# Optimization experiments

Hardware: AMD Instinct MI355X
Metric: run time of the kernel (lower is better)

The kernel has to match this reference:

```python
import jax, jax.numpy as jnp
import numpy as np

N_IN = 28
N_MID = 256
N_OUT = 28
SEQ = 28
BATCH = 4096


def setup_inputs() -> dict:
    key = jax.random.key(0)
    ks = jax.random.split(key, 8)
    s_ih = 1.0 / np.sqrt(N_MID)
    x = jax.random.normal(ks[0], (BATCH, SEQ, N_IN), dtype=jnp.float32)
    # PyTorch nn.GRU params: weight_ih_l0 [3H, in], weight_hh_l0 [3H, H], biases [3H]
    w_ih = jax.random.uniform(ks[1], (3 * N_MID, N_IN), minval=-s_ih, maxval=s_ih, dtype=jnp.float32)
    w_hh = jax.random.uniform(ks[2], (3 * N_MID, N_MID), minval=-s_ih, maxval=s_ih, dtype=jnp.float32)
    b_ih = jax.random.uniform(ks[3], (3 * N_MID,), minval=-s_ih, maxval=s_ih, dtype=jnp.float32)
    b_hh = jax.random.uniform(ks[4], (3 * N_MID,), minval=-s_ih, maxval=s_ih, dtype=jnp.float32)
    fc_w = jax.random.uniform(ks[5], (N_OUT, N_MID), minval=-s_ih, maxval=s_ih, dtype=jnp.float32)
    fc_b = jax.random.uniform(ks[6], (N_OUT,), minval=-s_ih, maxval=s_ih, dtype=jnp.float32)
    return {"x": x, "w_ih": w_ih, "w_hh": w_hh, "b_ih": b_ih, "b_hh": b_hh,
            "fc_w": fc_w, "fc_b": fc_b}


def _gru_last_hidden(x, w_ih, w_hh, b_ih, b_hh):
    B, T, _ = x.shape
    H = w_hh.shape[1]
    # Precompute input projection for all timesteps: [B, T, 3H]
    gi_all = jnp.einsum('bti,gi->btg', x, w_ih) + b_ih
    gi_all = jnp.moveaxis(gi_all, 1, 0)  # [T, B, 3H]

    def step(h, gi):
        gh = h @ w_hh.T + b_hh  # [B, 3H]
        i_r, i_z, i_n = jnp.split(gi, 3, axis=-1)
        h_r, h_z, h_n = jnp.split(gh, 3, axis=-1)
        r = jax.nn.sigmoid(i_r + h_r)
        z = jax.nn.sigmoid(i_z + h_z)
        n = jnp.tanh(i_n + r * h_n)
        h_new = (1.0 - z) * n + z * h
        return h_new, None

    h0 = jnp.zeros((B, H), dtype=x.dtype)
    h_last, _ = jax.lax.scan(step, h0, gi_all)
    return h_last


def reference(x, w_ih, w_hh, b_ih, b_hh, fc_w, fc_b):
    h_last = _gru_last_hidden(x, w_ih, w_hh, b_ih, b_hh)
    return h_last @ fc_w.T + fc_b
```

## Files before the change

### kernel.cpp

```cpp
#include <hip/hip_runtime.h>
#include <hip/hip_bf16.h>
#include <math.h>

#define N_IN 28
#define N_MID 256
#define N_OUT 28
#define SEQ 28
#define BATCH 4096
#define G3 768
#define ROWS 16
#define THREADS 512
#define NBLK (BATCH / ROWS)

#define LOG2E  1.44269504f
#define LOG2E2 2.88539008f

typedef __attribute__((ext_vector_type(8))) short bf16x8;
typedef __attribute__((ext_vector_type(4))) float f32x4;

#define MFMA(a, b, c) __builtin_amdgcn_mfma_f32_16x16x32_bf16((a), (b), (c), 0, 0, 0)

__device__ __forceinline__ f32x4 splat4(float v) {
    f32x4 r;
    r[0] = v; r[1] = v; r[2] = v; r[3] = v;
    return r;
}

__device__ __forceinline__ short f2bf(float v) {
    __hip_bfloat16 b = __float2bfloat16(v);
    return *reinterpret_cast<short*>(&b);
}
__device__ __forceinline__ float bf2f(short s) {
    unsigned int u = ((unsigned int)(unsigned short)s) << 16;
    return __uint_as_float(u);
}
__device__ __forceinline__ unsigned cvt_pk_bf16(float a, float b) {
    unsigned d;
    asm("v_cvt_pk_bf16_f32 %0, %1, %2" : "=v"(d) : "v"(a), "v"(b));
    return d;
}
__device__ __forceinline__ float frcp(float v) {
    return __builtin_amdgcn_rcpf(v);
}
__device__ __forceinline__ float fexp2(float v) {
#if __has_builtin(__builtin_amdgcn_exp2f)
    return __builtin_amdgcn_exp2f(v);
#else
    return __expf(v * 0.69314718f);
#endif
}
__device__ __forceinline__ float fsigmoid2(float v) {
    return frcp(1.0f + fexp2(-v));
}
__device__ __forceinline__ float ftanh2(float v) {
    return fmaf(-2.0f, frcp(1.0f + fexp2(v)), 1.0f);
}

__global__ void prep_w(const float* __restrict__ w_hh, const float* __restrict__ w_ih,
                       const float* __restrict__ b_ih, const float* __restrict__ b_hh,
                       short* __restrict__ wB, short* __restrict__ wI) {
    int idx = blockIdx.x * 256 + threadIdx.x;
    if (idx < G3 * N_MID) {
        int g = idx >> 8;
        float s = (g < 2 * N_MID) ? LOG2E : LOG2E2;
        wB[idx] = f2bf(w_hh[idx] * s);
    }
    if (idx < G3 * 32) {
        int g = idx >> 5, k = idx & 31;
        float s = (g < 2 * N_MID) ? LOG2E : LOG2E2;
        float v = 0.0f;
        if (k < N_IN) {
            v = w_ih[g * N_IN + k] * s;
        } else if (k == 28 || k == 29) {
            float bias = ((g < 2 * N_MID) ? (b_ih[g] + b_hh[g]) : b_ih[g]) * s;
            v = (k == 28) ? bias : (bias - bf2f(f2bf(bias)));
        }
        wI[idx] = f2bf(v);
    }
}

template<bool HID, int RB, bool LAST>
__device__ __forceinline__ void gru_step(
    int t, const float* __restrict__ x, int rowbase,
    int l15, int lg, int wv, int lane,
    short (&hl)[2][32][17][8],
    const short (&wlds)[2][3][16][64][8],
    const bf16x8 (&wreg)[3][2][6],
    const bf16x8 (&wireg)[3][2],
    const float (&bHN)[2],
    float (&hold)[2][4], const int (&colA)[2],
    float4 &xA, float4 &xB)
{
    constexpr int WB = RB ^ 1;

    float4 nA, nB;
    if (!LAST) {
        const float* xp =
            x + (size_t)(rowbase + l15) * (SEQ * N_IN) + (t + 1) * N_IN + lg * 8;
        nA = *(const float4*)xp;
        nB.x = 0.f; nB.y = 0.f; nB.z = 0.f; nB.w = 0.f;
        if (lg < 3) nB = *(const float4*)(xp + 4);
    }

    const f32x4 zero4 = splat4(0.0f);
    f32x4 aR[2], aZ[2], aIN[2], aHN[2];

    if constexpr (HID) {
        constexpr int ord[8] = {6, 7, 0, 1, 2, 3, 4, 5};
        bf16x8 ah2[2];
        ah2[0] = *(const bf16x8*)&hl[RB][ord[0] * 4 + lg][l15][0];
        __builtin_amdgcn_s_setprio(1);
        #pragma unroll
        for (int i = 0; i < 8; ++i) {
            const int ks = ord[i];
            const int cur = i & 1, nxt = cur ^ 1;
            if (i < 7)
                ah2[nxt] = *(const bf16x8*)&hl[RB][ord[i + 1] * 4 + lg][l15][0];
            #pragma unroll
            for (int a = 0; a < 2; ++a) {
                bf16x8 b0, b1, b2;
                if (ks < 6) {
                    b0 = wreg[0][a][ks]; b1 = wreg[1][a][ks]; b2 = wreg[2][a][ks];
                } else {
                    const int cg = 2 * wv + a;
                    b0 = *(const bf16x8*)&wlds[ks - 6][0][cg][lane][0];
                    b1 = *(const bf16x8*)&wlds[ks - 6][1][cg][lane][0];
                    b2 = *(const bf16x8*)&wlds[ks - 6][2][cg][lane][0];
                }
                if (i == 0) {
                    f32x4 cHN = splat4(bHN[a]);
                    aR[a]  = MFMA(ah2[cur], b0, zero4);
                    aZ[a]  = MFMA(ah2[cur], b1, zero4);
                    aHN[a] = MFMA(ah2[cur], b2, cHN);
                } else {
                    aR[a]  = MFMA(ah2[cur], b0, aR[a]);
                    aZ[a]  = MFMA(ah2[cur], b1, aZ[a]);
                    aHN[a] = MFMA(ah2[cur], b2, aHN[a]);
                }
            }
        }
        __builtin_amdgcn_s_setprio(0);
    }

    float xv[8] = {xA.x, xA.y, xA.z, xA.w, xB.x, xB.y, xB.z, xB.w};
    unsigned w0 = cvt_pk_bf16(xv[0], xv[1]);
    unsigned w1 = cvt_pk_bf16(xv[2], xv[3]);
    unsigned w2 = cvt_pk_bf16(xv[4], xv[5]);
    unsigned w3 = cvt_pk_bf16(xv[6], xv[7]);
    if (lg == 3) w2 = 0x3F803F80u;
    bf16x8 xh;
    {
        unsigned* xu = (unsigned*)&xh;
        xu[0] = w0; xu[1] = w1; xu[2] = w2; xu[3] = w3;
    }
    #pragma unroll
    for (int a = 0; a < 2; ++a) {
        if constexpr (HID) {
            aR[a]  = MFMA(xh, wireg[0][a], aR[a]);
            aZ[a]  = MFMA(xh, wireg[1][a], aZ[a]);
            aIN[a] = MFMA(xh, wireg[2][a], zero4);
        } else {
            aR[a]  = MFMA(xh, wireg[0][a], zero4);
            aZ[a]  = MFMA(xh, wireg[1][a], zero4);
            aIN[a] = MFMA(xh, wireg[2][a], zero4);
            aHN[a] = splat4(bHN[a]);
        }
    }

    #pragma unroll
    for (int a = 0; a < 2; ++a) {
        const int c = colA[a];
        float hn4[4];
        #pragma unroll
        for (int j = 0; j < 4; ++j) {
            float r = fsigmoid2(aR[a][j]);
            float z = fsigmoid2(aZ[a][j]);
            float n = ftanh2(aIN[a][j] + r * aHN[a][j]);
            float hnew = fmaf(z, hold[a][j] - n, n);
            hold[a][j] = hnew;
            hn4[j] = hnew;
        }
        unsigned p01 = cvt_pk_bf16(hn4[0], hn4[1]);
        unsigned p23 = cvt_pk_bf16(hn4[2], hn4[3]);
        short* bp = &hl[WB][c >> 3][4 * lg][c & 7];
        bp[0]  = (short)(p01 & 0xffffu);
        bp[8]  = (short)(p01 >> 16);
        bp[16] = (short)(p23 & 0xffffu);
        bp[24] = (short)(p23 >> 16);
    }

    if (!LAST) { xA = nA; xB = nB; }
    __syncthreads();
}

__global__ __launch_bounds__(THREADS, 2) void gru_onecu(
    const float* __restrict__ x,
    const short* __restrict__ wB,
    const short* __restrict__ wI,
    const float* __restrict__ b_hh,
    const float* __restrict__ fc_w,
    const float* __restrict__ fc_b,
    float* __restrict__ out)
{
    __shared__ short wlds[2][3][16][64][8];
    __shared__ short hl[2][32][17][8];

    const int tid  = threadIdx.x;
    const int lane = tid & 63;
    const int l15  = lane & 15;
    const int lg   = lane >> 4;
    const int wv   = tid >> 6;
    const int rowbase = blockIdx.x * ROWS;

    for (int idx = tid; idx < 2 * 3 * 16 * 64; idx += THREADS) {
        int L    = idx & 63;
        int frag = idx >> 6;
        int ksl  = frag / 48;
        int rem  = frag - ksl * 48;
        int g    = rem >> 4;
        int cg   = rem & 15;
        int col  = cg * 16 + (L & 15);
        int k0   = (6 + ksl) * 32 + (L >> 4) * 8;
        *(bf16x8*)&wlds[ksl][g][cg][L][0] =
            *(const bf16x8*)(wB + ((size_t)(g * 256 + col)) * 256 + k0);
    }

    bf16x8 wreg[3][2][6];
    bf16x8 wireg[3][2];
    int   colA[2];
    float bHN[2];
    #pragma unroll
    for (int a = 0; a < 2; ++a) {
        const int c = wv * 32 + a * 16 + l15;
        colA[a] = c;
        bHN[a]  = b_hh[512 + c] * LOG2E2;
        #pragma unroll
        for (int g = 0; g < 3; ++g) {
            wireg[g][a] = *(const bf16x8*)(wI + ((size_t)(g * 256 + c)) * 32 + lg * 8);
            #pragma unroll
            for (int ks = 0; ks < 6; ++ks)
                wreg[g][a][ks] =
                    *(const bf16x8*)(wB + ((size_t)(g * 256 + c)) * 256 + ks * 32 + lg * 8);
        }
    }

    float hold[2][4] = {};

    float4 xA, xB;
    {
        const float* xp = x + (size_t)(rowbase + l15) * (SEQ * N_IN) + lg * 8;
        xA = *(const float4*)xp;
        xB.x = 0.f; xB.y = 0.f; xB.z = 0.f; xB.w = 0.f;
        if (lg < 3) xB = *(const float4*)(xp + 4);
    }

    __syncthreads();

    gru_step<false, 0, false>(0, x, rowbase, l15, lg, wv, lane, hl, wlds, wreg,
                              wireg, bHN, hold, colA, xA, xB);
    for (int tt = 1; tt < SEQ - 1; tt += 2) {
        gru_step<true, 1, false>(tt, x, rowbase, l15, lg, wv, lane, hl, wlds, wreg,
                                 wireg, bHN, hold, colA, xA, xB);
        gru_step<true, 0, false>(tt + 1, x, rowbase, l15, lg, wv, lane, hl, wlds, wreg,
                                 wireg, bHN, hold, colA, xA, xB);
    }
    gru_step<true, 1, true>(SEQ - 1, x, rowbase, l15, lg, wv, lane, hl, wlds, wreg,
                            wireg, bHN, hold, colA, xA, xB);

    float* hf = (float*)&wlds[0][0][0][0][0];
    {
        int r = tid >> 5, kg = tid & 31;
        #pragma unroll
        for (int e = 0; e < 8; ++e) {
            int k = kg * 8 + e;
            hf[r * 256 + k] = bf2f(hl[0][k >> 3][r][k & 7]);
        }
    }
    __syncthreads();
    if (tid < ROWS * N_OUT) {
        int r = tid / N_OUT, o = tid - r * N_OUT;
        float acc = fc_b[o];
        #pragma unroll
        for (int k4 = 0; k4 < 64; ++k4) {
            float4 hv = *(const float4*)&hf[r * 256 + k4 * 4];
            float4 wv4 = *(const float4*)&fc_w[o * 256 + k4 * 4];
            acc = fmaf(hv.x, wv4.x, acc);
            acc = fmaf(hv.y, wv4.y, acc);
            acc = fmaf(hv.z, wv4.z, acc);
            acc = fmaf(hv.w, wv4.w, acc);
        }
        out[(size_t)(rowbase + r) * N_OUT + o] = acc;
    }
}

extern "C" void kernel_launch(void* const* d_in, const int* in_sizes, int n_in,
                              void* d_out, int out_size, void* d_ws, size_t ws_size,
                              hipStream_t stream) {
    const float* x    = (const float*)d_in[0];
    const float* w_ih = (const float*)d_in[1];
    const float* w_hh = (const float*)d_in[2];
    const float* b_ih = (const float*)d_in[3];
    const float* b_hh = (const float*)d_in[4];
    const float* fc_w = (const float*)d_in[5];
    const float* fc_b = (const float*)d_in[6];
    float* out = (float*)d_out;

    short* wB = (short*)d_ws;
    short* wI = wB + G3 * N_MID;

    hipLaunchKernelGGL(prep_w, dim3(768), dim3(256), 0, stream,
                       w_hh, w_ih, b_ih, b_hh, wB, wI);
    hipLaunchKernelGGL(gru_onecu, dim3(NBLK), dim3(THREADS), 0, stream,
                       x, wB, wI, b_hh, fc_w, fc_b, out);
}
```

Before: 77.16 us.

## Pre-convert inputs to padded time-major bf16 and issue input MFMAs first

```diff
diff --git a/kernel.cpp b/kernel.cpp
--- a/kernel.cpp
+++ b/kernel.cpp
@@ -79,9 +79,23 @@
     }
 }
 
+__global__ void prep_x(const float* __restrict__ x, short* __restrict__ xbf) {
+    int idx = blockIdx.x * 256 + threadIdx.x;
+    if (idx >= SEQ * BATCH * 32) return;
+    int k  = idx & 31;
+    int tb = idx >> 5;
+    int t  = tb >> 12;
+    int b  = tb & (BATCH - 1);
+    float v;
+    if (k < N_IN)            v = x[(size_t)b * (SEQ * N_IN) + t * N_IN + k];
+    else if (k == 28 || k == 29) v = 1.0f;
+    else                     v = 0.0f;
+    xbf[idx] = f2bf(v);
+}
+
 template<bool HID, int RB, bool LAST>
 __device__ __forceinline__ void gru_step(
-    int t, const float* __restrict__ x, int rowbase,
+    int t, const short* __restrict__ xbf, int rowbase,
     int l15, int lg, int wv, int lane,
     short (&hl)[2][32][17][8],
     const short (&wlds)[2][3][16][64][8],
@@ -89,26 +103,32 @@
     const bf16x8 (&wireg)[3][2],
     const float (&bHN)[2],
     float (&hold)[2][4], const int (&colA)[2],
-    float4 &xA, float4 &xB)
+    bf16x8 &xh)
 {
     constexpr int WB = RB ^ 1;
 
-    float4 nA, nB;
-    if (!LAST) {
-        const float* xp =
-            x + (size_t)(rowbase + l15) * (SEQ * N_IN) + (t + 1) * N_IN + lg * 8;
-        nA = *(const float4*)xp;
-        nB.x = 0.f; nB.y = 0.f; nB.z = 0.f; nB.w = 0.f;
-        if (lg < 3) nB = *(const float4*)(xp + 4);
-    }
+    bf16x8 nxh;
+    if (!LAST)
+        nxh = *(const bf16x8*)(xbf +
+              ((size_t)(t + 1) * BATCH + rowbase + l15) * 32 + lg * 8);
 
     const f32x4 zero4 = splat4(0.0f);
     f32x4 aR[2], aZ[2], aIN[2], aHN[2];
 
+    constexpr int ord[8] = {6, 7, 0, 1, 2, 3, 4, 5};
+    bf16x8 ah2[2];
+    if constexpr (HID)
+        ah2[0] = *(const bf16x8*)&hl[RB][ord[0] * 4 + lg][l15][0];
+
+    #pragma unroll
+    for (int a = 0; a < 2; ++a) {
+        aR[a]  = MFMA(xh, wireg[0][a], zero4);
+        aZ[a]  = MFMA(xh, wireg[1][a], zero4);
+        aIN[a] = MFMA(xh, wireg[2][a], zero4);
+        if constexpr (!HID) aHN[a] = splat4(bHN[a]);
+    }
+
     if constexpr (HID) {
-        constexpr int ord[8] = {6, 7, 0, 1, 2, 3, 4, 5};
-        bf16x8 ah2[2];
-        ah2[0] = *(const bf16x8*)&hl[RB][ord[0] * 4 + lg][l15][0];
         __builtin_amdgcn_s_setprio(1);
         #pragma unroll
         for (int i = 0; i < 8; ++i) {
@@ -127,44 +147,16 @@
                     b1 = *(const bf16x8*)&wlds[ks - 6][1][cg][lane][0];
                     b2 = *(const bf16x8*)&wlds[ks - 6][2][cg][lane][0];
                 }
+                aR[a] = MFMA(ah2[cur], b0, aR[a]);
+                aZ[a] = MFMA(ah2[cur], b1, aZ[a]);
                 if (i == 0) {
-                    f32x4 cHN = splat4(bHN[a]);
-                    aR[a]  = MFMA(ah2[cur], b0, zero4);
-                    aZ[a]  = MFMA(ah2[cur], b1, zero4);
-                    aHN[a] = MFMA(ah2[cur], b2, cHN);
+                    aHN[a] = MFMA(ah2[cur], b2, splat4(bHN[a]));
                 } else {
-                    aR[a]  = MFMA(ah2[cur], b0, aR[a]);
-                    aZ[a]  = MFMA(ah2[cur], b1, aZ[a]);
                     aHN[a] = MFMA(ah2[cur], b2, aHN[a]);
                 }
             }
         }
         __builtin_amdgcn_s_setprio(0);
-    }
-
-    float xv[8] = {xA.x, xA.y, xA.z, xA.w, xB.x, xB.y, xB.z, xB.w};
-    unsigned w0 = cvt_pk_bf16(xv[0], xv[1]);
-    unsigned w1 = cvt_pk_bf16(xv[2], xv[3]);
-    unsigned w2 = cvt_pk_bf16(xv[4], xv[5]);
-    unsigned w3 = cvt_pk_bf16(xv[6], xv[7]);
-    if (lg == 3) w2 = 0x3F803F80u;
-    bf16x8 xh;
-    {
-        unsigned* xu = (unsigned*)&xh;
-        xu[0] = w0; xu[1] = w1; xu[2] = w2; xu[3] = w3;
-    }
-    #pragma unroll
-    for (int a = 0; a < 2; ++a) {
-        if constexpr (HID) {
-            aR[a]  = MFMA(xh, wireg[0][a], aR[a]);
-            aZ[a]  = MFMA(xh, wireg[1][a], aZ[a]);
-            aIN[a] = MFMA(xh, wireg[2][a], zero4);
-        } else {
-            aR[a]  = MFMA(xh, wireg[0][a], zero4);
-            aZ[a]  = MFMA(xh, wireg[1][a], zero4);
-            aIN[a] = MFMA(xh, wireg[2][a], zero4);
-            aHN[a] = splat4(bHN[a]);
-        }
     }
 
     #pragma unroll
@@ -189,12 +181,12 @@
         bp[24] = (short)(p23 >> 16);
     }
 
-    if (!LAST) { xA = nA; xB = nB; }
+    if (!LAST) xh = nxh;
     __syncthreads();
 }
 
 __global__ __launch_bounds__(THREADS, 2) void gru_onecu(
-    const float* __restrict__ x,
+    const short* __restrict__ xbf,
     const short* __restrict__ wB,
     const short* __restrict__ wI,
     const float* __restrict__ b_hh,
@@ -246,26 +238,20 @@
 
     float hold[2][4] = {};
 
-    float4 xA, xB;
-    {
-        const float* xp = x + (size_t)(rowbase + l15) * (SEQ * N_IN) + lg * 8;
-        xA = *(const float4*)xp;
-        xB.x = 0.f; xB.y = 0.f; xB.z = 0.f; xB.w = 0.f;
-        if (lg < 3) xB = *(const float4*)(xp + 4);
-    }
+    bf16x8 xh = *(const bf16x8*)(xbf + ((size_t)(rowbase + l15)) * 32 + lg * 8);
 
     __syncthreads();
 
-    gru_step<false, 0, false>(0, x, rowbase, l15, lg, wv, lane, hl, wlds, wreg,
-                              wireg, bHN, hold, colA, xA, xB);
+    gru_step<false, 0, false>(0, xbf, rowbase, l15, lg, wv, lane, hl, wlds, wreg,
+                              wireg, bHN, hold, colA, xh);
     for (int tt = 1; tt < SEQ - 1; tt += 2) {
-        gru_step<true, 1, false>(tt, x, rowbase, l15, lg, wv, lane, hl, wlds, wreg,
-                                 wireg, bHN, hold, colA, xA, xB);
-        gru_step<true, 0, false>(tt + 1, x, rowbase, l15, lg, wv, lane, hl, wlds, wreg,
-                                 wireg, bHN, hold, colA, xA, xB);
-    }
-    gru_step<true, 1, true>(SEQ - 1, x, rowbase, l15, lg, wv, lane, hl, wlds, wreg,
-                            wireg, bHN, hold, colA, xA, xB);
+        gru_step<true, 1, false>(tt, xbf, rowbase, l15, lg, wv, lane, hl, wlds,
+                                 wreg, wireg, bHN, hold, colA, xh);
+        gru_step<true, 0, false>(tt + 1, xbf, rowbase, l15, lg, wv, lane, hl, wlds,
+                                 wreg, wireg, bHN, hold, colA, xh);
+    }
+    gru_step<true, 1, true>(SEQ - 1, xbf, rowbase, l15, lg, wv, lane, hl, wlds,
+                            wreg, wireg, bHN, hold, colA, xh);
 
     float* hf = (float*)&wlds[0][0][0][0][0];
     {
@@ -305,11 +291,14 @@
     const float* fc_b = (const float*)d_in[6];
     float* out = (float*)d_out;
 
-    short* wB = (short*)d_ws;
-    short* wI = wB + G3 * N_MID;
+    short* wB  = (short*)d_ws;
+    short* wI  = wB + G3 * N_MID;
+    short* xbf = wI + G3 * 32;
 
     hipLaunchKernelGGL(prep_w, dim3(768), dim3(256), 0, stream,
                        w_hh, w_ih, b_ih, b_hh, wB, wI);
+    hipLaunchKernelGGL(prep_x, dim3((SEQ * BATCH * 32 + 255) / 256), dim3(256),
+                       0, stream, x, xbf);
     hipLaunchKernelGGL(gru_onecu, dim3(NBLK), dim3(THREADS), 0, stream,
-                       x, wB, wI, b_hh, fc_w, fc_b, out);
-}
+                       xbf, wB, wI, b_hh, fc_w, fc_b, out);
+}
```

After: 80.56 us. 1.04x slower.
